# Kernel tuning notes

Measured on AMD Instinct MI355X. Metric: run time of the kernel, lower is better.

Reference implementation:

```python
import jax, jax.numpy as jnp
import numpy as np

W_DIM = 512
FREQ = 1024
CH = 512
OUT_CH = 512
SIZE = 64
SR = 64.0
BW = 2.0
MAX_BW = BW * 8.0
B = 16
K = 3


def setup_inputs() -> dict:
    key = jax.random.key(0)
    ks = jax.random.split(key, 10)
    w = jax.random.normal(ks[0], (B, W_DIM), dtype=jnp.float32)
    # SynthesisInput buffers: random unit-direction freqs scaled by uniform radius in [0, max_bw)
    f = jax.random.normal(ks[1], (FREQ, 2), dtype=jnp.float32)
    f = f / jnp.linalg.norm(f, axis=1, keepdims=True)
    freqs = f * (jax.random.uniform(ks[2], (FREQ, 1), dtype=jnp.float32) * MAX_BW)
    phases = jax.random.uniform(ks[3], (FREQ,), dtype=jnp.float32) - 0.5
    input_weight = jax.random.normal(ks[4], (CH, FREQ), dtype=jnp.float32)
    # affine: FullyConnectedLayer(w_dim, 4, weight_init=0, bias_init=[1,0,0,0])
    affine_w = jnp.zeros((4, W_DIM), dtype=jnp.float32)
    affine_b = jnp.array([1.0, 0.0, 0.0, 0.0], dtype=jnp.float32)
    # per-layer style affine (w -> in_channels), bias_init=1 (StyleGAN convention)
    style_w = jax.random.normal(ks[5], (CH, W_DIM), dtype=jnp.float32)
    style_b = jnp.ones((CH,), dtype=jnp.float32)
    conv_w = jax.random.normal(ks[6], (OUT_CH, CH, K, K), dtype=jnp.float32)
    conv_b = jnp.zeros((OUT_CH,), dtype=jnp.float32)
    return {"w": w, "affine_w": affine_w, "affine_b": affine_b, "freqs": freqs,
            "phases": phases, "input_weight": input_weight, "style_w": style_w,
            "style_b": style_b, "conv_w": conv_w, "conv_b": conv_b}


def _fc(x, weight, bias):
    # FullyConnectedLayer: weight_gain = 1/sqrt(in_features)
    gain = 1.0 / np.sqrt(weight.shape[1])
    return x @ (weight * gain).T + bias


def _synthesis_input(w, affine_w, affine_b, freqs, phases, input_weight):
    t = _fc(w, affine_w, affine_b)                                  # [B,4]
    t = t / jnp.linalg.norm(t[:, :2], axis=1, keepdims=True)
    c, s, tx, ty = t[:, 0], t[:, 1], t[:, 2], t[:, 3]
    # m = m_r @ m_t (only the 2x3 top block matters)
    rot = jnp.stack([jnp.stack([c, -s], -1), jnp.stack([s, c], -1)], 1)  # [B,2,2]
    trans = jnp.stack([-tx, -ty], -1)                               # [B,2]
    shift = jnp.einsum('bij,bj->bi', rot, trans)                    # [B,2]
    phases_b = phases[None, :] + jnp.einsum('fi,bi->bf', freqs, shift)
    freqs_b = jnp.einsum('fi,bij->bfj', freqs, rot)                 # [B,F,2]
    amp = jnp.clip(1.0 - (jnp.linalg.norm(freqs_b, axis=2) - BW) / (SR / 2.0 - BW), 0.0, 1.0)
    # affine_grid(theta=diag(0.5*size/sr)=0.5, align_corners=False)
    theta00 = 0.5 * SIZE / SR
    xs = ((jnp.arange(SIZE, dtype=jnp.float32) + 0.5) / SIZE * 2.0 - 1.0) * theta00
    ys = ((jnp.arange(SIZE, dtype=jnp.float32) + 0.5) / SIZE * 2.0 - 1.0) * theta00
    gx, gy = jnp.meshgrid(xs, ys)                                   # [H,W]
    grid = jnp.stack([gx, gy], axis=-1)                             # [H,W,2]
    x = jnp.einsum('hwi,bfi->bhwf', grid, freqs_b) + phases_b[:, None, None, :]
    x = jnp.sin(x * (2.0 * np.pi)) * amp[:, None, None, :]
    effect_freq = jnp.sum((jnp.linalg.norm(freqs, axis=-1) < BW).astype(jnp.float32))
    x = jnp.einsum('bhwf,cf->bchw', x, input_weight / jnp.sqrt(effect_freq))
    return x                                                        # [B,CH,H,W]


def _modulated_conv2d(x, weight, s, padding=1):
    # demodulate: pre-normalize w and s
    w_hat = weight * jax.lax.rsqrt(jnp.mean(jnp.square(weight), axis=(1, 2, 3), keepdims=True))
    s_hat = s * jax.lax.rsqrt(jnp.mean(jnp.square(s)))
    # dcoefs[b,o] = rsqrt(sum_ikl (w[o,i,k,l]*s[b,i])^2 + eps)
    dcoefs = jax.lax.rsqrt(jnp.einsum('oikl,bi->bo', jnp.square(w_hat), jnp.square(s_hat)) + 1e-8)
    # grouped-per-sample conv == scale input channels by s, conv with base w, scale out by dcoefs
    x = x * s_hat[:, :, None, None]
    y = jax.lax.conv_general_dilated(x, w_hat, window_strides=(1, 1),
                                     padding=[(padding, padding), (padding, padding)],
                                     dimension_numbers=('NCHW', 'OIHW', 'NCHW'))
    return y * dcoefs[:, :, None, None]


def reference(w, affine_w, affine_b, freqs, phases, input_weight, style_w, style_b, conv_w, conv_b):
    x = _synthesis_input(w, affine_w, affine_b, freqs, phases, input_weight)
    s = _fc(w, style_w, style_b)                                    # [B,CH]
    y = _modulated_conv2d(x, conv_w, s, padding=K // 2)
    y = y + conv_b[None, :, None, None]
    y = jnp.where(y >= 0, y, 0.2 * y) * np.sqrt(2.0)                # lrelu + gain (bias_act)
    y = jnp.clip(y, -256.0, 256.0)                                  # conv_clamp
    return y
```

## Files before the change

### kernel.cpp

```cpp
#include <hip/hip_runtime.h>

typedef __attribute__((ext_vector_type(4))) float f32x4;
typedef __attribute__((ext_vector_type(8))) __bf16 bf16x8;

__device__ __forceinline__ unsigned short f2bf(float f) {
  unsigned int u = __builtin_bit_cast(unsigned int, f);
  return (unsigned short)((u + 0x7FFFu + ((u >> 16) & 1u)) >> 16);
}

__device__ __forceinline__ float sin2pi(float x) {
#if __has_builtin(__builtin_amdgcn_sinf) && __has_builtin(__builtin_amdgcn_fractf)
  return __builtin_amdgcn_sinf(__builtin_amdgcn_fractf(x));
#else
  return __sinf(x * 6.283185307179586f);
#endif
}

__device__ __forceinline__ void gll16(const void* g, void* l) {
  __builtin_amdgcn_global_load_lds(
      (const __attribute__((address_space(1))) void*)g,
      (__attribute__((address_space(3))) void*)l, 16, 0, 0);
}

template <int W>
__device__ __forceinline__ void vmwait() {
  if constexpr (W == 0) asm volatile("s_waitcnt vmcnt(0)" ::: "memory");
  else if constexpr (W == 2) asm volatile("s_waitcnt vmcnt(2)" ::: "memory");
  else if constexpr (W == 4) asm volatile("s_waitcnt vmcnt(4)" ::: "memory");
  else if constexpr (W == 6) asm volatile("s_waitcnt vmcnt(6)" ::: "memory");
  else if constexpr (W == 8) asm volatile("s_waitcnt vmcnt(8)" ::: "memory");
}

#define CFENCE() asm volatile("" ::: "memory")

__global__ void prep_freq_k(const float* __restrict__ w, const float* __restrict__ affine_w,
                            const float* __restrict__ affine_b, const float* __restrict__ freqs,
                            const float* __restrict__ phases, float4* __restrict__ freq_data,
                            float* __restrict__ scal) {
  const int b = blockIdx.x, tid = threadIdx.x;
  const int wv = tid >> 6, lane = tid & 63;
  __shared__ float tdot[4];
  __shared__ float par[4];
  __shared__ float scnt;
  float sum = 0.f;
  for (int i = lane; i < 512; i += 64) sum += w[b * 512 + i] * affine_w[wv * 512 + i];
#pragma unroll
  for (int o = 32; o > 0; o >>= 1) sum += __shfl_down(sum, o);
  if (lane == 0) tdot[wv] = sum;
  if (tid == 0) scnt = 0.f;
  __syncthreads();
  if (tid == 0) {
    const float gain = 0.04419417382415922f;
    float t0 = tdot[0] * gain + affine_b[0];
    float t1 = tdot[1] * gain + affine_b[1];
    float t2 = tdot[2] * gain + affine_b[2];
    float t3 = tdot[3] * gain + affine_b[3];
    float inv = 1.f / sqrtf(t0 * t0 + t1 * t1);
    float c = t0 * inv, s = t1 * inv, tx = t2 * inv, ty = t3 * inv;
    par[0] = c; par[1] = s;
    par[2] = -c * tx + s * ty;
    par[3] = -s * tx - c * ty;
  }
  __syncthreads();
  const float c = par[0], s = par[1], sh0 = par[2], sh1 = par[3];
  float cnt = 0.f;
  for (int f = tid; f < 1024; f += 256) {
    float fx = freqs[2 * f], fy = freqs[2 * f + 1];
    float fb0 = fx * c + fy * s;
    float fb1 = fy * c - fx * s;
    float ph = phases[f] + fx * sh0 + fy * sh1;
    float nb = sqrtf(fb0 * fb0 + fb1 * fb1);
    float amp = fminf(fmaxf(1.f - (nb - 2.f) * (1.f / 30.f), 0.f), 1.f);
    float4 v; v.x = fb0; v.y = fb1; v.z = ph; v.w = amp;
    freq_data[(b << 10) + f] = v;
    if (sqrtf(fx * fx + fy * fy) < 2.f) cnt += 1.f;
  }
  if (b == 0) {
    atomicAdd(&scnt, cnt);
    __syncthreads();
    if (tid == 0) scal[0] = 1.f / sqrtf(scnt);
  }
}

__global__ void style_k(const float* __restrict__ w, const float* __restrict__ style_w,
                        const float* __restrict__ style_b, float* __restrict__ s_out) {
  int idx = blockIdx.x * 256 + threadIdx.x;
  int b = idx >> 9, c = idx & 511;
  const float gain = 0.04419417382415922f;
  const float4* wr = (const float4*)(w + b * 512);
  const float4* sr = (const float4*)(style_w + (size_t)c * 512);
  float sum = 0.f;
#pragma unroll 4
  for (int i = 0; i < 128; ++i) {
    float4 a = wr[i], q = sr[i];
    sum += a.x * q.x + a.y * q.y + a.z * q.z + a.w * q.w;
  }
  s_out[idx] = sum * gain + style_b[c];
}

__global__ void convw_prep_k(const float* __restrict__ conv_w, float* __restrict__ wsumT,
                             unsigned short* __restrict__ bt_conv) {
  const int o = blockIdx.x, tid = threadIdx.x;
  __shared__ float red[256];
  float sum = 0.f;
  for (int i = tid; i < 4608; i += 256) { float v = conv_w[o * 4608 + i]; sum += v * v; }
  red[tid] = sum;
  __syncthreads();
  for (int off = 128; off > 0; off >>= 1) {
    if (tid < off) red[tid] += red[tid + off];
    __syncthreads();
  }
  const float rn = rsqrtf(red[0] * (1.f / 4608.f));
  for (int i = tid; i < 512; i += 256) {
    float sq = 0.f;
#pragma unroll
    for (int kl = 0; kl < 9; ++kl) {
      float v = conv_w[(o * 512 + i) * 9 + kl];
      sq += v * v;
      bt_conv[o * 4608 + kl * 512 + i] = f2bf(v * rn);
    }
    wsumT[i * 512 + o] = sq * rn * rn;
  }
}

__global__ void iw_cast_k(const float* __restrict__ iw, unsigned short* __restrict__ iw_bf) {
  int i = blockIdx.x * 256 + threadIdx.x;
  iw_bf[i] = f2bf(iw[i]);
}

__global__ void shat_dcoef_k(const float* __restrict__ s, const float* __restrict__ wsumT,
                             float* __restrict__ s_hat, float* __restrict__ dcoefs) {
  const int b = blockIdx.x, tid = threadIdx.x;
  __shared__ float red[256];
  __shared__ float sh2[512];
  float sum = 0.f;
  for (int i = tid; i < 8192; i += 256) { float v = s[i]; sum += v * v; }
  red[tid] = sum;
  __syncthreads();
  for (int off = 128; off > 0; off >>= 1) {
    if (tid < off) red[tid] += red[tid + off];
    __syncthreads();
  }
  const float inv_rms = rsqrtf(red[0] * (1.f / 8192.f));
  for (int c = tid; c < 512; c += 256) {
    float sh = s[b * 512 + c] * inv_rms;
    s_hat[b * 512 + c] = sh;
    sh2[c] = sh * sh;
  }
  __syncthreads();
  for (int o = tid; o < 512; o += 256) {
    float acc = 0.f;
    for (int i = 0; i < 512; ++i) acc += wsumT[i * 512 + o] * sh2[i];
    dcoefs[b * 512 + o] = rsqrtf(acc + 1e-8f);
  }
}

__global__ void border_zero_k(unsigned short* __restrict__ xmp) {
  int idx = blockIdx.x * 256 + threadIdx.x;
  int chunk = idx & 63;
  int t = idx >> 6;
  int p = t % 260;
  int b = t / 260;
  int h, w;
  if (p < 66) { h = 0; w = p; }
  else if (p < 132) { h = 65; w = p - 66; }
  else if (p < 196) { h = p - 131; w = 0; }
  else { h = p - 195; w = 65; }
  uint4 z; z.x = 0; z.y = 0; z.z = 0; z.w = 0;
  *(uint4*)&xmp[(((size_t)b * 66 + h) * 66 + w) * 512 + chunk * 8] = z;
}

__device__ __forceinline__ void sy_sgB(char* lB, const unsigned short* iw, int n0, int d,
                                       int rb, int kt, int lane, int lsw) {
  const unsigned short* src = iw + (size_t)(n0 + rb + (lane >> 3)) * 1024 + (kt << 6) + lsw;
  gll16(src, lB + d * 32768 + rb * 128);
}

__global__ __launch_bounds__(256, 2) void synth_gemm2_k(
    const float4* __restrict__ freq_data, const unsigned short* __restrict__ iw_bf,
    const float* __restrict__ s_hat, const float* __restrict__ scal,
    unsigned short* __restrict__ xmp) {
  extern __shared__ char sl[];
  char* lA = sl;
  char* lB = sl + 16384;
  const int bid = blockIdx.x;
  const int mt = bid >> 1, nt = bid & 1;
  const int m0 = mt << 7, n0 = nt << 8;
  const int b = m0 >> 12;
  const int hbase = (m0 >> 6) & 63;
  const int tid = threadIdx.x, lane = tid & 63, wv = tid >> 6;
  const int wm = (wv >> 1) << 6, wn = (wv & 1) << 7;
  const int g = tid & 15;
  const int r0 = (tid >> 4) << 3;
  const int lsw = (((lane & 7) ^ (lane >> 3)) << 3);
  const int aswz = (((lane >> 4) << 4)) ^ ((lane & 7) << 4);
  const char* pA = lA + (size_t)(wm + (lane & 15)) * 128;
  const int browB = wn + (lane & 15);
  f32x4 acc[4][8];
#pragma unroll
  for (int mi = 0; mi < 4; ++mi)
#pragma unroll
    for (int ni = 0; ni < 8; ++ni) { f32x4 z = {0.f, 0.f, 0.f, 0.f}; acc[mi][ni] = z; }
  const float gy0 = (hbase + 0.5f) * 0.015625f - 0.5f;
  const float gy1 = (hbase + 1.5f) * 0.015625f - 0.5f;

#pragma unroll
  for (int ig = 0; ig < 8; ++ig) sy_sgB(lB, iw_bf, n0, 0, wv * 64 + ig * 8, 0, lane, lsw);
  vmwait<0>();
  __builtin_amdgcn_s_barrier();
  CFENCE();

  for (int kt = 0; kt < 16; ++kt) {
    if (kt < 15) {
#pragma unroll
      for (int ig = 0; ig < 8; ++ig)
        sy_sgB(lB, iw_bf, n0, (kt + 1) & 1, wv * 64 + ig * 8, kt + 1, lane, lsw);
    }
    const float4* fdp = freq_data + (b << 10) + (kt << 6) + (g << 2);
    float4 fd0 = fdp[0], fd1 = fdp[1], fd2 = fdp[2], fd3 = fdp[3];
#pragma unroll
    for (int j = 0; j < 8; ++j) {
      const int r = r0 + j;
      const float gx = ((r & 63) + 0.5f) * 0.015625f - 0.5f;
      const float gy = (r >> 6) ? gy1 : gy0;
      ushort4 u;
      u.x = f2bf(sin2pi(gx * fd0.x + gy * fd0.y + fd0.z) * fd0.w);
      u.y = f2bf(sin2pi(gx * fd1.x + gy * fd1.y + fd1.z) * fd1.w);
      u.z = f2bf(sin2pi(gx * fd2.x + gy * fd2.y + fd2.z) * fd2.w);
      u.w = f2bf(sin2pi(gx * fd3.x + gy * fd3.y + fd3.z) * fd3.w);
      *(ushort4*)(lA + r * 128 + ((g << 3) ^ (j << 4))) = u;
    }
    asm volatile("s_waitcnt lgkmcnt(0)" ::: "memory");
    if (kt < 15) vmwait<8>(); else vmwait<0>();
    __builtin_amdgcn_s_barrier();
    CFENCE();
    __builtin_amdgcn_sched_barrier(0);

    const char* pB = lB + ((kt & 1) << 15) + (size_t)browB * 128;
#pragma unroll
    for (int ks = 0; ks < 2; ++ks) {
      const int ao = aswz ^ (ks << 6);
      bf16x8 af[4], bq[8];
#pragma unroll
      for (int mi = 0; mi < 4; ++mi) af[mi] = *(const bf16x8*)(pA + mi * 2048 + ao);
#pragma unroll
      for (int ni = 0; ni < 8; ++ni) bq[ni] = *(const bf16x8*)(pB + ni * 2048 + ao);
      __builtin_amdgcn_s_setprio(1);
#pragma unroll
      for (int mi = 0; mi < 4; ++mi)
#pragma unroll
        for (int ni = 0; ni < 8; ++ni)
          acc[mi][ni] = __builtin_amdgcn_mfma_f32_16x16x32_bf16(af[mi], bq[ni], acc[mi][ni], 0, 0, 0);
      __builtin_amdgcn_s_setprio(0);
    }
    CFENCE();
    __builtin_amdgcn_s_barrier();
    CFENCE();
  }

  const float inv_eff = scal[0];
  const int c_lo = lane & 15, r_hi = (lane >> 4) << 2;
#pragma unroll
  for (int ni = 0; ni < 8; ++ni) {
    const int cc = n0 + wn + (ni << 4) + c_lo;
    const float sc = s_hat[b * 512 + cc] * inv_eff;
#pragma unroll
    for (int mi = 0; mi < 4; ++mi) {
#pragma unroll
      for (int j = 0; j < 4; ++j) {
        const int rr = wm + (mi << 4) + r_hi + j;
        const int hp = hbase + (rr >> 6) + 1;
        const int wp = (rr & 63) + 1;
        xmp[(((size_t)b * 66 + hp) * 66 + wp) * 512 + cc] = f2bf(acc[mi][ni][j] * sc);
      }
    }
  }
}

__device__ __forceinline__ float epi_act(float a, float dco, float cb) {
  float y = a * dco + cb;
  y = (y >= 0.f ? y : 0.2f * y) * 1.4142135623730951f;
  return fminf(fmaxf(y, -256.f), 256.f);
}

struct ConvCtx {
  const unsigned short* xmp;
  const unsigned short* bt;
  int n0, hb, b_img, lane;
  int lsw;
  int gB_rb0;
  int gA_lo;
  int gA_up;
};

__device__ __forceinline__ void tile_geom(int t, int& dh, int& dw, int& kc, int& koff) {
  const int kc8 = t / 9;
  const int off = t - 9 * kc8;
  dh = off / 3;
  dw = off - 3 * dh;
  kc = kc8 << 6;
  koff = off * 512 + kc;
}

__device__ __forceinline__ void sgA(char* lds, const ConvCtx& c, int d, int rb,
                                    int dh, int dw, int kc) {
  const int r = rb + (c.lane >> 3);
  const int h = c.hb + (r >> 6) + dh;
  const int w = (r & 63) + dw;
  const unsigned short* src = c.xmp + (((size_t)c.b_img * 66 + h) * 66 + w) * 512 + kc + c.lsw;
  gll16(src, lds + d * 32768 + rb * 128);
}

__device__ __forceinline__ void sgB(char* lds, const ConvCtx& c, int d, int rb, int koff) {
  const int row = c.n0 + rb + (c.lane >> 3);
  const unsigned short* src = c.bt + (size_t)row * 4608 + koff + c.lsw;
  gll16(src, lds + 65536 + d * 32768 + rb * 128);
}

template <bool STG>
__device__ __forceinline__ void conv_tile1(char* lds, const ConvCtx& c, f32x4 (&acc)[8][4],
                                           const char* pA, const char* pB, int aswz0, int t) {
  int dh1, dw1, kc1, koff1;
  tile_geom(t + 1, dh1, dw1, kc1, koff1);
  const int D = t & 1, Dn = D ^ 1;
  const int db = D << 15;
  const int a0 = aswz0, a1 = aswz0 ^ 64;

  vmwait<0>();
  __builtin_amdgcn_s_barrier();
  CFENCE();
  __builtin_amdgcn_sched_barrier(0);

  bf16x8 bq[4], af[4];
#pragma unroll
  for (int ni = 0; ni < 4; ++ni) bq[ni] = *(const bf16x8*)(pB + db + ni * 2048 + a0);
#pragma unroll
  for (int i = 0; i < 4; ++i) af[i] = *(const bf16x8*)(pA + db + i * 2048 + a0);
  if (STG) {
    sgB(lds, c, Dn, c.gB_rb0, koff1);      sgB(lds, c, Dn, c.gB_rb0 + 8, koff1);
    sgB(lds, c, Dn, c.gB_rb0 + 16, koff1); sgB(lds, c, Dn, c.gB_rb0 + 24, koff1);
  }
  __builtin_amdgcn_s_setprio(1);
#pragma unroll
  for (int i = 0; i < 4; ++i)
#pragma unroll
    for (int ni = 0; ni < 4; ++ni)
      acc[i][ni] = __builtin_amdgcn_mfma_f32_16x16x32_bf16(af[i], bq[ni], acc[i][ni], 0, 0, 0);
  __builtin_amdgcn_s_setprio(0);
#pragma unroll
  for (int i = 0; i < 4; ++i) af[i] = *(const bf16x8*)(pA + db + (4 + i) * 2048 + a0);
  if (STG) {
    sgA(lds, c, Dn, c.gA_up, dh1, dw1, kc1); sgA(lds, c, Dn, c.gA_up + 8, dh1, dw1, kc1);
    sgA(lds, c, Dn, c.gA_lo, dh1, dw1, kc1); sgA(lds, c, Dn, c.gA_lo + 8, dh1, dw1, kc1);
  }
  __builtin_amdgcn_s_setprio(1);
#pragma unroll
  for (int i = 0; i < 4; ++i)
#pragma unroll
    for (int ni = 0; ni < 4; ++ni)
      acc[4 + i][ni] = __builtin_amdgcn_mfma_f32_16x16x32_bf16(af[i], bq[ni], acc[4 + i][ni], 0, 0, 0);
  __builtin_amdgcn_s_setprio(0);
#pragma unroll
  for (int ni = 0; ni < 4; ++ni) bq[ni] = *(const bf16x8*)(pB + db + ni * 2048 + a1);
#pragma unroll
  for (int i = 0; i < 4; ++i) af[i] = *(const bf16x8*)(pA + db + i * 2048 + a1);
  __builtin_amdgcn_s_setprio(1);
#pragma unroll
  for (int i = 0; i < 4; ++i)
#pragma unroll
    for (int ni = 0; ni < 4; ++ni)
      acc[i][ni] = __builtin_amdgcn_mfma_f32_16x16x32_bf16(af[i], bq[ni], acc[i][ni], 0, 0, 0);
  __builtin_amdgcn_s_setprio(0);
#pragma unroll
  for (int i = 0; i < 4; ++i) af[i] = *(const bf16x8*)(pA + db + (4 + i) * 2048 + a1);
  __builtin_amdgcn_s_setprio(1);
#pragma unroll
  for (int i = 0; i < 4; ++i)
#pragma unroll
    for (int ni = 0; ni < 4; ++ni)
      acc[4 + i][ni] = __builtin_amdgcn_mfma_f32_16x16x32_bf16(af[i], bq[ni], acc[4 + i][ni], 0, 0, 0);
  __builtin_amdgcn_s_setprio(0);
  CFENCE();
}

__global__ __launch_bounds__(512, 2) void conv_gemm8_k(
    const unsigned short* __restrict__ xmp, const unsigned short* __restrict__ bt_conv,
    const float* __restrict__ dcoefs, const float* __restrict__ conv_b,
    float* __restrict__ out) {
  extern __shared__ char lds[];
  const int tid = threadIdx.x, lane = tid & 63, wv = tid >> 6;
  const int bid = blockIdx.x;
  const int wg = (bid & 7) * 64 + (bid >> 3);
  const int mt = wg >> 1, nt = wg & 1;
  const int m0 = mt << 8, n0 = nt << 8;
  const int b_img = m0 >> 12;
  const int hb = (m0 >> 6) & 63;
  const int wm = (wv >> 2) << 7, wn = (wv & 3) << 6;

  ConvCtx c;
  c.xmp = xmp; c.bt = bt_conv;
  c.n0 = n0; c.hb = hb; c.b_img = b_img; c.lane = lane;
  c.lsw = (((lane & 7) ^ (lane >> 3)) << 3);
  c.gB_rb0 = (((wv & 3) >> 1) << 7) + (((wv & 1) | ((wv >> 2) << 1)) << 5);
  c.gA_lo = wm + ((wv & 3) << 4);
  c.gA_up = c.gA_lo + 64;

  const char* pA = lds + (size_t)(wm + (lane & 15)) * 128;
  const char* pB = lds + 65536 + (size_t)(wn + (lane & 15)) * 128;
  const int aswz0 = (((lane >> 4) << 4)) ^ ((lane & 7) << 4);

  f32x4 acc[8][4];
#pragma unroll
  for (int mi = 0; mi < 8; ++mi)
#pragma unroll
    for (int ni = 0; ni < 4; ++ni) { f32x4 z = {0.f, 0.f, 0.f, 0.f}; acc[mi][ni] = z; }

  sgB(lds, c, 0, c.gB_rb0, 0);       sgB(lds, c, 0, c.gB_rb0 + 8, 0);
  sgB(lds, c, 0, c.gB_rb0 + 16, 0);  sgB(lds, c, 0, c.gB_rb0 + 24, 0);
  sgA(lds, c, 0, c.gA_up, 0, 0, 0);  sgA(lds, c, 0, c.gA_up + 8, 0, 0, 0);
  sgA(lds, c, 0, c.gA_lo, 0, 0, 0);  sgA(lds, c, 0, c.gA_lo + 8, 0, 0, 0);

  for (int t = 0; t < 71; ++t) conv_tile1<true>(lds, c, acc, pA, pB, aswz0, t);
  conv_tile1<false>(lds, c, acc, pA, pB, aswz0, 71);

  const int c_lo = lane & 15, r_hi = (lane >> 4) << 2;
#pragma unroll
  for (int ni = 0; ni < 4; ++ni) {
    const int oo = n0 + wn + (ni << 4) + c_lo;
    const float dco = dcoefs[b_img * 512 + oo];
    const float cb = conv_b[oo];
#pragma unroll
    for (int mi = 0; mi < 8; ++mi) {
      const int rr = wm + (mi << 4) + r_hi;
      const int hh = hb + (rr >> 6);
      const int w0 = rr & 63;
      float4 v;
      v.x = epi_act(acc[mi][ni][0], dco, cb);
      v.y = epi_act(acc[mi][ni][1], dco, cb);
      v.z = epi_act(acc[mi][ni][2], dco, cb);
      v.w = epi_act(acc[mi][ni][3], dco, cb);
      *(float4*)&out[(((size_t)b_img * 512 + oo) * 64 + hh) * 64 + w0] = v;
    }
  }
}

extern "C" void kernel_launch(void* const* d_in, const int* in_sizes, int n_in,
                              void* d_out, int out_size, void* d_ws, size_t ws_size,
                              hipStream_t stream) {
  (void)in_sizes; (void)n_in; (void)out_size;
  const float* w        = (const float*)d_in[0];
  const float* affine_w = (const float*)d_in[1];
  const float* affine_b = (const float*)d_in[2];
  const float* freqs    = (const float*)d_in[3];
  const float* phases   = (const float*)d_in[4];
  const float* input_weight = (const float*)d_in[5];
  const float* style_w  = (const float*)d_in[6];
  const float* style_b  = (const float*)d_in[7];
  const float* conv_w   = (const float*)d_in[8];
  const float* conv_b   = (const float*)d_in[9];
  float* out = (float*)d_out;

  char* p = (char*)d_ws;
  float4* freq_data = (float4*)p;               p += (size_t)16 * 1024 * 16;
  float* scal = (float*)p;                      p += 256;
  float* s_buf = (float*)p;                     p += 8192 * 4;
  float* s_hat = (float*)p;                     p += 8192 * 4;
  float* wsumT = (float*)p;                     p += (size_t)512 * 512 * 4;
  float* dcoefs = (float*)p;                    p += 8192 * 4;
  unsigned short* iw_bf = (unsigned short*)p;   p += (size_t)512 * 1024 * 2;
  unsigned short* bt_conv = (unsigned short*)p; p += (size_t)512 * 4608 * 2;
  unsigned short* xmp = (unsigned short*)p;     p += (size_t)16 * 66 * 66 * 512 * 2;
  if (ws_size < (size_t)(p - (char*)d_ws)) return;

  (void)hipFuncSetAttribute((const void*)conv_gemm8_k,
                            hipFuncAttributeMaxDynamicSharedMemorySize, 131072);
  (void)hipFuncSetAttribute((const void*)synth_gemm2_k,
                            hipFuncAttributeMaxDynamicSharedMemorySize, 81920);

  border_zero_k<<<1040, 256, 0, stream>>>(xmp);
  prep_freq_k<<<16, 256, 0, stream>>>(w, affine_w, affine_b, freqs, phases, freq_data, scal);
  style_k<<<32, 256, 0, stream>>>(w, style_w, style_b, s_buf);
  convw_prep_k<<<512, 256, 0, stream>>>(conv_w, wsumT, bt_conv);
  iw_cast_k<<<2048, 256, 0, stream>>>(input_weight, iw_bf);
  shat_dcoef_k<<<16, 256, 0, stream>>>(s_buf, wsumT, s_hat, dcoefs);
  synth_gemm2_k<<<1024, 256, 81920, stream>>>(freq_data, iw_bf, s_hat, scal, xmp);
  conv_gemm8_k<<<512, 512, 131072, stream>>>(xmp, bt_conv, dcoefs, conv_b, out);
}
```

Before: 418.1 us.

## Compute full N per block in synth GEMM, loading B directly into registers

The synthesis GEMM now has each 512-thread block cover all 512 output channels for a 128-row M tile, so the sinusoidal A tile is computed once per tile instead of twice. The B operand (input_weight in bf16) is loaded straight from global memory into registers rather than double-buffered through LDS. Block IDs are swizzled to group tiles across CUs. This removes the redundant sin evaluations and the LDS traffic for B. In exchange it adds register pressure, issues uncoalesced per-lane global B loads with no prefetch overlap, and halves the block count.

```diff
diff --git a/kernel.cpp b/kernel.cpp
--- a/kernel.cpp
+++ b/kernel.cpp
@@ -170,32 +170,24 @@
   *(uint4*)&xmp[(((size_t)b * 66 + h) * 66 + w) * 512 + chunk * 8] = z;
 }
 
-__device__ __forceinline__ void sy_sgB(char* lB, const unsigned short* iw, int n0, int d,
-                                       int rb, int kt, int lane, int lsw) {
-  const unsigned short* src = iw + (size_t)(n0 + rb + (lane >> 3)) * 1024 + (kt << 6) + lsw;
-  gll16(src, lB + d * 32768 + rb * 128);
-}
-
-__global__ __launch_bounds__(256, 2) void synth_gemm2_k(
+__global__ __launch_bounds__(512, 2) void synth_gemm3_k(
     const float4* __restrict__ freq_data, const unsigned short* __restrict__ iw_bf,
     const float* __restrict__ s_hat, const float* __restrict__ scal,
     unsigned short* __restrict__ xmp) {
-  extern __shared__ char sl[];
-  char* lA = sl;
-  char* lB = sl + 16384;
+  __shared__ __align__(16) char lA[16384];
   const int bid = blockIdx.x;
-  const int mt = bid >> 1, nt = bid & 1;
-  const int m0 = mt << 7, n0 = nt << 8;
+  const int wg = (bid & 7) * 64 + (bid >> 3);
+  const int m0 = wg << 7;
   const int b = m0 >> 12;
   const int hbase = (m0 >> 6) & 63;
   const int tid = threadIdx.x, lane = tid & 63, wv = tid >> 6;
-  const int wm = (wv >> 1) << 6, wn = (wv & 1) << 7;
-  const int g = tid & 15;
-  const int r0 = (tid >> 4) << 3;
-  const int lsw = (((lane & 7) ^ (lane >> 3)) << 3);
+  const int wm = (wv >> 2) << 6;
+  const int wn = (wv & 3) << 7;
+  const int g = tid & 31;
+  const int r0 = (tid >> 5) << 3;
   const int aswz = (((lane >> 4) << 4)) ^ ((lane & 7) << 4);
   const char* pA = lA + (size_t)(wm + (lane & 15)) * 128;
-  const int browB = wn + (lane & 15);
+  const unsigned short* Bp = iw_bf + (size_t)(wn + (lane & 15)) * 1024 + ((lane >> 4) << 3);
   f32x4 acc[4][8];
 #pragma unroll
   for (int mi = 0; mi < 4; ++mi)
@@ -204,53 +196,44 @@
   const float gy0 = (hbase + 0.5f) * 0.015625f - 0.5f;
   const float gy1 = (hbase + 1.5f) * 0.015625f - 0.5f;
 
-#pragma unroll
-  for (int ig = 0; ig < 8; ++ig) sy_sgB(lB, iw_bf, n0, 0, wv * 64 + ig * 8, 0, lane, lsw);
-  vmwait<0>();
-  __builtin_amdgcn_s_barrier();
-  CFENCE();
-
   for (int kt = 0; kt < 16; ++kt) {
-    if (kt < 15) {
-#pragma unroll
-      for (int ig = 0; ig < 8; ++ig)
-        sy_sgB(lB, iw_bf, n0, (kt + 1) & 1, wv * 64 + ig * 8, kt + 1, lane, lsw);
-    }
-    const float4* fdp = freq_data + (b << 10) + (kt << 6) + (g << 2);
-    float4 fd0 = fdp[0], fd1 = fdp[1], fd2 = fdp[2], fd3 = fdp[3];
+    bf16x8 bq0[8], bq1[8];
+#pragma unroll
+    for (int ni = 0; ni < 8; ++ni) {
+      bq0[ni] = *(const bf16x8*)(Bp + (size_t)ni * 16384 + (kt << 6));
+      bq1[ni] = *(const bf16x8*)(Bp + (size_t)ni * 16384 + (kt << 6) + 32);
+    }
+    __builtin_amdgcn_sched_barrier(0);
+    const float4* fdp = freq_data + (b << 10) + (kt << 6) + (g << 1);
+    float4 fd0 = fdp[0], fd1 = fdp[1];
 #pragma unroll
     for (int j = 0; j < 8; ++j) {
       const int r = r0 + j;
       const float gx = ((r & 63) + 0.5f) * 0.015625f - 0.5f;
       const float gy = (r >> 6) ? gy1 : gy0;
-      ushort4 u;
+      ushort2 u;
       u.x = f2bf(sin2pi(gx * fd0.x + gy * fd0.y + fd0.z) * fd0.w);
       u.y = f2bf(sin2pi(gx * fd1.x + gy * fd1.y + fd1.z) * fd1.w);
-      u.z = f2bf(sin2pi(gx * fd2.x + gy * fd2.y + fd2.z) * fd2.w);
-      u.w = f2bf(sin2pi(gx * fd3.x + gy * fd3.y + fd3.z) * fd3.w);
-      *(ushort4*)(lA + r * 128 + ((g << 3) ^ (j << 4))) = u;
+      *(ushort2*)(lA + r * 128 + ((g << 2) ^ ((r & 7) << 4))) = u;
     }
     asm volatile("s_waitcnt lgkmcnt(0)" ::: "memory");
-    if (kt < 15) vmwait<8>(); else vmwait<0>();
     __builtin_amdgcn_s_barrier();
     CFENCE();
     __builtin_amdgcn_sched_barrier(0);
 
-    const char* pB = lB + ((kt & 1) << 15) + (size_t)browB * 128;
 #pragma unroll
     for (int ks = 0; ks < 2; ++ks) {
       const int ao = aswz ^ (ks << 6);
-      bf16x8 af[4], bq[8];
+      bf16x8 af[4];
 #pragma unroll
       for (int mi = 0; mi < 4; ++mi) af[mi] = *(const bf16x8*)(pA + mi * 2048 + ao);
-#pragma unroll
-      for (int ni = 0; ni < 8; ++ni) bq[ni] = *(const bf16x8*)(pB + ni * 2048 + ao);
       __builtin_amdgcn_s_setprio(1);
 #pragma unroll
       for (int mi = 0; mi < 4; ++mi)
 #pragma unroll
         for (int ni = 0; ni < 8; ++ni)
-          acc[mi][ni] = __builtin_amdgcn_mfma_f32_16x16x32_bf16(af[mi], bq[ni], acc[mi][ni], 0, 0, 0);
+          acc[mi][ni] = __builtin_amdgcn_mfma_f32_16x16x32_bf16(
+              af[mi], ks ? bq1[ni] : bq0[ni], acc[mi][ni], 0, 0, 0);
       __builtin_amdgcn_s_setprio(0);
     }
     CFENCE();
@@ -262,7 +245,7 @@
   const int c_lo = lane & 15, r_hi = (lane >> 4) << 2;
 #pragma unroll
   for (int ni = 0; ni < 8; ++ni) {
-    const int cc = n0 + wn + (ni << 4) + c_lo;
+    const int cc = wn + (ni << 4) + c_lo;
     const float sc = s_hat[b * 512 + cc] * inv_eff;
 #pragma unroll
     for (int mi = 0; mi < 4; ++mi) {
@@ -474,8 +457,6 @@
 
   (void)hipFuncSetAttribute((const void*)conv_gemm8_k,
                             hipFuncAttributeMaxDynamicSharedMemorySize, 131072);
-  (void)hipFuncSetAttribute((const void*)synth_gemm2_k,
-                            hipFuncAttributeMaxDynamicSharedMemorySize, 81920);
 
   border_zero_k<<<1040, 256, 0, stream>>>(xmp);
   prep_freq_k<<<16, 256, 0, stream>>>(w, affine_w, affine_b, freqs, phases, freq_data, scal);
@@ -483,6 +464,6 @@
   convw_prep_k<<<512, 256, 0, stream>>>(conv_w, wsumT, bt_conv);
   iw_cast_k<<<2048, 256, 0, stream>>>(input_weight, iw_bf);
   shat_dcoef_k<<<16, 256, 0, stream>>>(s_buf, wsumT, s_hat, dcoefs);
-  synth_gemm2_k<<<1024, 256, 81920, stream>>>(freq_data, iw_bf, s_hat, scal, xmp);
+  synth_gemm3_k<<<512, 512, 0, stream>>>(freq_data, iw_bf, s_hat, scal, xmp);
   conv_gemm8_k<<<512, 512, 131072, stream>>>(xmp, bt_conv, dcoefs, conv_b, out);
 }
```

Result: slower. 503.3 us (+20.4%).
